# Optimization experiments

Measured on AMD Instinct MI355X. Metric: run time of the kernel, lower is better.

The kernel has to match this reference:

```python
import jax, jax.numpy as jnp
from jax import lax
import numpy as np

B = 32  # batch


def _conv(x, w, b, pad):
    # x: [B,Cin,H,W], w: [Cout,Cin,kh,kw], b: [Cout]
    y = lax.conv_general_dilated(x, w, window_strides=(1, 1), padding=pad,
                                 dimension_numbers=("NCHW", "OIHW", "NCHW"))
    return y + b[None, :, None, None]


def setup_inputs() -> dict:
    keys = jax.random.split(jax.random.key(0), 16)
    ki = iter(keys)
    f32 = jnp.float32

    def W(shape):
        return jax.random.normal(next(ki), shape, f32) * 0.05

    return {
        "x": jax.random.normal(next(ki), (B, 64, 64), f32),
        # 64 independent spatial convs per stage, each Conv2d(Cin,31,(64,3))
        "W1": W((64, 31, 1, 64, 3)),  "b1": jnp.zeros((64, 31), f32),
        "W2": W((64, 31, 31, 64, 3)), "b2": jnp.zeros((64, 31), f32),
        "W3": W((64, 31, 31, 64, 3)), "b3": jnp.zeros((64, 31), f32),
        # 2 edge spectral stacks: Conv(2,64,9)->ReLU->Conv(64,32,1)->ReLU->Conv(32,1,5)
        "We1a": W((2, 64, 2, 9, 9)),  "be1a": jnp.zeros((2, 64), f32),
        "We1b": W((2, 32, 64, 1, 1)), "be1b": jnp.zeros((2, 32), f32),
        "We1c": W((2, 1, 32, 5, 5)),  "be1c": jnp.zeros((2, 1), f32),
        # 29 interior spectral stacks: Conv(3,64,9)->ReLU->Conv(64,32,1)->ReLU->Conv(32,1,5)
        "We2a": W((29, 64, 3, 9, 9)),  "be2a": jnp.zeros((29, 64), f32),
        "We2b": W((29, 32, 64, 1, 1)), "be2b": jnp.zeros((29, 32), f32),
        "We2c": W((29, 1, 32, 5, 5)),  "be2c": jnp.zeros((29, 1), f32),
    }


def _spatial(inp, Ws, bs):
    # inp: [B,Cin,64,64]; Ws: [64,31,Cin,64,3]; bs: [64,31]
    def one(w, b):
        return jax.nn.relu(_conv(inp, w, b, [(0, 0), (1, 1)]))  # [B,31,1,64]
    rows = jax.vmap(one)(Ws, bs)            # [64,B,31,1,64]; row i = output line i
    return jnp.transpose(rows[:, :, :, 0, :], (1, 2, 0, 3))  # [B,31,64,64]


def _spectral(xin, wa, ba, wb, bb, wc, bc):
    h = jax.nn.relu(_conv(xin, wa, ba, [(4, 4), (4, 4)]))
    h = jax.nn.relu(_conv(h, wb, bb, [(0, 0), (0, 0)]))
    return _conv(h, wc, bc, [(2, 2), (2, 2)])[:, 0]  # [B,64,64]


def reference(x, W1, b1, W2, b2, W3, b3,
              We1a, be1a, We1b, be1b, We1c, be1c,
              We2a, be2a, We2b, be2b, We2c, be2c):
    xb = x[:, None]                         # [B,1,64,64]
    s1 = _spatial(xb, W1, b1)               # [B,31,64,64]
    s2 = _spatial(s1, W2, b2)
    s3 = _spatial(s2, W3, b3)

    # edge bands 0 and 30 use 2-channel slices
    edge_in = jnp.stack([s3[:, 0:2], s3[:, 29:31]])   # [2,B,2,64,64]
    edge = jax.vmap(_spectral)(edge_in, We1a, be1a, We1b, be1b, We1c, be1c)  # [2,B,64,64]

    # interior bands 1..29 use sliding 3-channel slices
    idx = jnp.arange(29)[:, None] + jnp.arange(3)[None, :]  # [29,3]
    mid_in = jnp.transpose(s3[:, idx], (1, 0, 2, 3, 4))     # [29,B,3,64,64]
    mid = jax.vmap(_spectral)(mid_in, We2a, be2a, We2b, be2b, We2c, be2c)  # [29,B,64,64]

    recon = jnp.concatenate(
        [edge[0][:, None], jnp.transpose(mid, (1, 0, 2, 3)), edge[1][:, None]], axis=1)
    out = s3 + recon                        # [B,31,64,64]
    # torch: .transpose(3,1).transpose(2,1) == permute(0,2,3,1)
    return jnp.transpose(out, (0, 2, 3, 1))  # [B,64,64,31]
```

## Files before the change

kernel.cpp:

```cpp
#include <hip/hip_runtime.h>
#include <hip/hip_bf16.h>
#include <stdint.h>

typedef unsigned short u16;
typedef unsigned int   u32;
typedef __attribute__((ext_vector_type(8))) short bf16x8;
typedef __attribute__((ext_vector_type(4))) float f32x4;

__device__ __forceinline__ float us2f(u16 u){ return __uint_as_float(((u32)u)<<16); }
__device__ __forceinline__ float lo2f(u32 w){ return __uint_as_float(w<<16); }
__device__ __forceinline__ float hi2f(u32 w){ return __uint_as_float(w & 0xffff0000u); }
__device__ __forceinline__ u16 f2us(float f){
  u32 u = __float_as_uint(f);
  u32 r = (u + 0x7FFFu + ((u>>16)&1u)) >> 16;
  return (u16)r;
}
__device__ __forceinline__ u32 pk2(float a, float b){ return (u32)f2us(a) | ((u32)f2us(b)<<16); }

__global__ __launch_bounds__(256) void k_prep_x(const float* __restrict__ x, u16* __restrict__ xT){
  __shared__ float tile[64][65];
  const int b = blockIdx.x, t = threadIdx.x;
  #pragma unroll
  for (int q=0;q<4;q++){
    int idx = q*256 + t, r = idx>>4, w4 = (idx&15)*4;
    float4 v = *(const float4*)&x[((size_t)b*64 + r)*64 + w4];
    tile[r][w4]=v.x; tile[r][w4+1]=v.y; tile[r][w4+2]=v.z; tile[r][w4+3]=v.w;
  }
  __syncthreads();
  #pragma unroll
  for (int q=0;q<2;q++){
    int idx = q*256 + t, w = idx>>3, rc = idx&7;
    uint4 o;
    o.x = pk2(tile[rc*8+0][w], tile[rc*8+1][w]);
    o.y = pk2(tile[rc*8+2][w], tile[rc*8+3][w]);
    o.z = pk2(tile[rc*8+4][w], tile[rc*8+5][w]);
    o.w = pk2(tile[rc*8+6][w], tile[rc*8+7][w]);
    *(uint4*)&xT[((size_t)b*64 + w)*64 + rc*8] = o;
  }
}

__global__ __launch_bounds__(256) void k_prep_w(const float* __restrict__ W,
        u16* __restrict__ Wp, int CI){
  __shared__ float rowW[5952];
  const int h = blockIdx.x, i = blockIdx.y, t = threadIdx.x;
  for (int idx=t; idx<1488; idx+=256){
    int o = idx/48, j4 = (idx - o*48)*4;
    float4 v = *(const float4*)&W[ (((size_t)h*31 + o)*CI + i)*192 + j4 ];
    *(float4*)&rowW[o*192 + j4] = v;
  }
  __syncthreads();
  for (int idx=t; idx<768; idx+=256){
    int dw = idx>>8, rem = idx&255, o = rem>>3, rc = rem&7;
    uint4 ov = {0,0,0,0};
    if (o < 31){
      const float* s = &rowW[o*192 + dw];
      ov.x = pk2(s[(rc*8+0)*3], s[(rc*8+1)*3]);
      ov.y = pk2(s[(rc*8+2)*3], s[(rc*8+3)*3]);
      ov.z = pk2(s[(rc*8+4)*3], s[(rc*8+5)*3]);
      ov.w = pk2(s[(rc*8+6)*3], s[(rc*8+7)*3]);
    }
    *(uint4*)&Wp[ ((((size_t)h*CI + i)*3 + dw)*32 + o)*64 + rc*8 ] = ov;
  }
}

__global__ __launch_bounds__(128) void k_spatial2(const u16* __restrict__ inT_g,
        const u16* __restrict__ Wp, const float* __restrict__ bias,
        float* __restrict__ outF, u16* __restrict__ outT, int CI, int mode){
  __shared__ __align__(16) u16 inT[2][66*72];
  const int t    = threadIdx.x;
  const int wv   = t>>6;
  const int lane = t&63;
  const int l15  = lane&15;
  const int quad = lane>>4;
  const int b    = blockIdx.x;
  const int hg   = blockIdx.y;
  const int h    = hg*2 + wv;

  if (t < 72){
    inT[0][t] = 0; inT[0][65*72 + t] = 0;
    inT[1][t] = 0; inT[1][65*72 + t] = 0;
  }

  f32x4 acc[2][4];
  #pragma unroll
  for (int n=0;n<2;n++)
    #pragma unroll
    for (int ms=0;ms<4;ms++) acc[n][ms] = (f32x4){0.f,0.f,0.f,0.f};

  const uint4* srcb = (const uint4*)(inT_g + (size_t)b*CI*4096);

  uint4 pf[4];
  #pragma unroll
  for (int q=0;q<4;q++) pf[q] = srcb[q*128 + t];

  for (int i=0;i<CI;i++){
    u16* L = inT[i&1];
    #pragma unroll
    for (int q=0;q<4;q++){
      int idx = q*128 + t, row = idx>>3, ch = idx&7;
      *(uint4*)&L[(row+1)*72 + ch*8] = pf[q];
    }
    if (i+1 < CI){
      const uint4* src = srcb + (size_t)(i+1)*512;
      #pragma unroll
      for (int q=0;q<4;q++) pf[q] = src[q*128 + t];
    }
    const u16* wbase = Wp + ((size_t)h*CI + i)*3*32*64;
    bf16x8 bfr[2][3][2];
    #pragma unroll
    for (int dw=0;dw<3;dw++)
      #pragma unroll
      for (int n=0;n<2;n++)
        #pragma unroll
        for (int kh=0;kh<2;kh++)
          bfr[kh][dw][n] = *(const bf16x8*)&wbase[(dw*32 + n*16 + l15)*64 + kh*32 + quad*8];
    asm volatile("s_waitcnt lgkmcnt(0)" ::: "memory");
    __builtin_amdgcn_s_barrier();
    __builtin_amdgcn_sched_barrier(0);
    #pragma unroll
    for (int kh=0; kh<2; kh++){
      #pragma unroll
      for (int dw=0; dw<3; dw++){
        bf16x8 afr[4];
        #pragma unroll
        for (int ms=0;ms<4;ms++)
          afr[ms] = *(const bf16x8*)&L[(ms*16 + l15 + dw)*72 + kh*32 + quad*8];
        #pragma unroll
        for (int n=0;n<2;n++)
          #pragma unroll
          for (int ms=0;ms<4;ms++)
            acc[n][ms] = __builtin_amdgcn_mfma_f32_16x16x32_bf16(afr[ms], bfr[kh][dw][n], acc[n][ms], 0,0,0);
      }
    }
  }
  #pragma unroll
  for (int n=0;n<2;n++){
    int o = n*16 + l15;
    if (o < 31){
      float bv = bias[h*31 + o];
      if (mode == 0){
        #pragma unroll
        for (int ms=0;ms<4;ms++){
          size_t base = (((size_t)b*31 + o)*64 + h)*64 + ms*16 + quad*4;
          #pragma unroll
          for (int reg=0;reg<4;reg++)
            outF[base + reg] = fmaxf(acc[n][ms][reg] + bv, 0.f);
        }
      } else {
        #pragma unroll
        for (int ms=0;ms<4;ms++){
          int w0 = ms*16 + quad*4;
          #pragma unroll
          for (int reg=0;reg<4;reg++)
            outT[ (((size_t)b*31 + o)*64 + (w0+reg))*64 + h ] = f2us(fmaxf(acc[n][ms][reg] + bv, 0.f));
        }
      }
    }
  }
}

__global__ __launch_bounds__(256) void k_prep(
    const float* __restrict__ We1a, const float* __restrict__ We2a,
    const float* __restrict__ We1b, const float* __restrict__ We2b,
    u16* __restrict__ waP, u16* __restrict__ wbP){
  int t = blockIdx.x*256 + threadIdx.x;
  if (t < 17856){
    int g = t/576, rem = t - g*576, dx = rem>>6, c = rem&63;
    int C; const float* wa;
    if (g==0)      { C=2; wa = We1a; }
    else if (g==30){ C=2; wa = We1a + 64*2*81; }
    else           { C=3; wa = We2a + (size_t)(g-1)*64*3*81; }
    const float* wrow = wa + (size_t)c*C*81;
    u16* dst = waP + ((size_t)(g*9 + dx)*64 + c)*40;
    int Kr = C*9;
    for (int k=0;k<40;k++){
      u16 v = 0;
      if (k < Kr) v = f2us(wrow[k*9 + dx]);
      dst[k] = v;
    }
  } else if (t < 17856 + 992){
    int u = t - 17856; int g = u>>5, c2 = u&31;
    const float* wb;
    if (g==0)      wb = We1b;
    else if (g==30) wb = We1b + 32*64;
    else            wb = We2b + (size_t)(g-1)*32*64;
    u16* dst = wbP + ((size_t)g*32 + c2)*72;
    for (int k=0;k<64;k++) dst[k] = f2us(wb[c2*64 + k]);
    for (int k=64;k<72;k++) dst[k] = 0;
  }
}

__global__ __launch_bounds__(256) void k_spec_ab(
    const float* __restrict__ s3,
    const u16* __restrict__ waP, const u16* __restrict__ wbP,
    const float* __restrict__ be1a, const float* __restrict__ be1b,
    const float* __restrict__ be2a, const float* __restrict__ be2b,
    u16* __restrict__ hb, int g0){
  __shared__ __align__(16) unsigned char smem[36864];
  u16* colT = (u16*)smem;
  u16* haT  = (u16*)smem;
  u16* hbL  = (u16*)smem;

  const int t = threadIdx.x;
  const int yo = blockIdx.x, b = blockIdx.y;
  const int gl = blockIdx.z;
  const int g  = g0 + gl;
  const int y0 = yo*4;
  const int wv = t>>6, lane = t&63, l15 = lane&15, quad = lane>>4;

  int C, cb; const float *ba, *bb;
  if (g==0)      { C=2; cb=0;  ba=be1a;           bb=be1b;        }
  else if (g==30){ C=2; cb=29; ba=be1a+64;        bb=be1b+32;     }
  else           { C=3; cb=g-1; ba=be2a+(size_t)(g-1)*64; bb=be2b+(size_t)(g-1)*32; }

  {
    uint4 z = {0,0,0,0};
    uint4* c4 = (uint4*)colT;
    #pragma unroll
    for (int j=0;j<6;j++){ int idx = j*256 + t; if (idx < 1440) c4[idx] = z; }
  }
  __syncthreads();

  for (int idx=t; idx<576; idx+=256){
    int i = idx/192, rem = idx-192*i;
    int x4 = rem/12, yext = rem - x4*12;
    int yrow = y0 + yext - 4;
    if (i < C && yrow >= 0 && yrow < 64){
      float4 v = *(const float4*)&s3[ (((size_t)b*31 + cb + i)*64 + yrow)*64 + x4*4 ];
      u16 q0=f2us(v.x), q1=f2us(v.y), q2=f2us(v.z), q3=f2us(v.w);
      #pragma unroll
      for (int yl=0; yl<4; yl++){
        int dy = yext - yl;
        if (dy >= 0 && dy < 9){
          int k = i*9 + dy;
          int base = (yl*72 + x4*4 + 4)*40 + k;
          colT[base      ] = q0;
          colT[base + 40 ] = q1;
          colT[base + 80 ] = q2;
          colT[base + 120] = q3;
        }
      }
    }
  }
  __syncthreads();

  f32x4 acc[4][4];
  #pragma unroll
  for (int yl=0;yl<4;yl++)
    #pragma unroll
    for (int nf=0;nf<4;nf++) acc[yl][nf] = (f32x4){0.f,0.f,0.f,0.f};

  const u16* waPg = waP + (size_t)g*9*64*40;
  #pragma unroll
  for (int dx=0; dx<9; dx++){
    bf16x8 af[4];
    #pragma unroll
    for (int yl=0;yl<4;yl++)
      af[yl] = *(const bf16x8*)&colT[(yl*72 + wv*16 + l15 + dx)*40 + quad*8];
    #pragma unroll
    for (int nf=0;nf<4;nf++){
      bf16x8 bfr = *(const bf16x8*)&waPg[(dx*64 + nf*16 + l15)*40 + quad*8];
      #pragma unroll
      for (int yl=0;yl<4;yl++)
        acc[yl][nf] = __builtin_amdgcn_mfma_f32_16x16x32_bf16(af[yl], bfr, acc[yl][nf], 0,0,0);
    }
  }
  __syncthreads();

  #pragma unroll
  for (int nf=0;nf<4;nf++){
    float bav = ba[nf*16 + l15];
    #pragma unroll
    for (int yl=0;yl<4;yl++){
      int px = yl*64 + wv*16 + quad*4;
      #pragma unroll
      for (int reg=0;reg<4;reg++)
        haT[(px+reg)*72 + nf*16 + l15] = f2us(fmaxf(acc[yl][nf][reg] + bav, 0.f));
    }
  }
  __syncthreads();

  bf16x8 a2[2][4];
  #pragma unroll
  for (int kh=0; kh<2; kh++)
    #pragma unroll
    for (int j=0;j<4;j++)
      a2[kh][j] = *(const bf16x8*)&haT[((wv*4+j)*16 + l15)*72 + kh*32 + quad*8];
  __syncthreads();

  const u16* wb_g = wbP + (size_t)g*32*72;
  f32x4 acc2[4][2];
  #pragma unroll
  for (int j=0;j<4;j++){ acc2[j][0] = (f32x4){0.f,0.f,0.f,0.f}; acc2[j][1] = (f32x4){0.f,0.f,0.f,0.f}; }
  #pragma unroll
  for (int kh=0; kh<2; kh++){
    #pragma unroll
    for (int nf=0;nf<2;nf++){
      bf16x8 b2 = *(const bf16x8*)&wb_g[(nf*16 + l15)*72 + kh*32 + quad*8];
      #pragma unroll
      for (int j=0;j<4;j++)
        acc2[j][nf] = __builtin_amdgcn_mfma_f32_16x16x32_bf16(a2[kh][j], b2, acc2[j][nf], 0,0,0);
    }
  }
  #pragma unroll
  for (int nf=0;nf<2;nf++){
    float bbv = bb[nf*16 + l15];
    #pragma unroll
    for (int j=0;j<4;j++){
      int px = (wv*4+j)*16 + quad*4;
      uint2 pw;
      pw.x = pk2(fmaxf(acc2[j][nf][0] + bbv, 0.f), fmaxf(acc2[j][nf][1] + bbv, 0.f));
      pw.y = pk2(fmaxf(acc2[j][nf][2] + bbv, 0.f), fmaxf(acc2[j][nf][3] + bbv, 0.f));
      *(uint2*)&hbL[(nf*16+l15)*296 + px] = pw;
    }
  }
  __syncthreads();

  {
    int c2 = t>>3, xq = t&7;
    size_t base = (((size_t)gl*32 + b)*32 + c2)*4096 + (size_t)yo*256 + xq*32;
    #pragma unroll
    for (int q=0;q<4;q++)
      *(uint4*)&hb[base + q*8] = *(const uint4*)&hbL[c2*296 + xq*32 + q*8];
  }
}

__global__ __launch_bounds__(256) void k_spec_c(
    const u16* __restrict__ hb, const float* __restrict__ We1c, const float* __restrict__ be1c,
    const float* __restrict__ We2c, const float* __restrict__ be2c,
    float* __restrict__ rec, int g0){
  __shared__ __align__(16) unsigned char smemC[58368 + 3200];
  u16*   hbT  = (u16*)smemC;
  float* wcL  = (float*)(smemC + 58368);
  float* redc = (float*)smemC;
  const int t  = threadIdx.x;
  const int y0 = blockIdx.x*8;
  const int b  = blockIdx.y;
  const int gl = blockIdx.z;
  const int g  = g0 + gl;
  const float *wc, *bc;
  if (g==0)      { wc = We1c;             bc = be1c;       }
  else if (g==30){ wc = We1c + 800;       bc = be1c + 1;   }
  else           { wc = We2c + (g-1)*800; bc = be2c + (g-1); }

  for (int idx=t; idx<384; idx+=256){
    int c2 = idx/12, row = idx - c2*12;
    u32* d32 = (u32*)&hbT[(size_t)(c2*12 + row)*76];
    d32[0]  = 0;
    d32[33] = 0;
    u32* di = d32 + 1;
    int yg = y0 - 2 + row;
    if (yg >= 0 && yg < 64){
      const uint4* srcp = (const uint4*)&hb[ (((size_t)gl*32 + b)*32 + c2)*4096 + (size_t)yg*64 ];
      #pragma unroll
      for (int q=0;q<8;q++){
        uint4 v = srcp[q];
        di[q*4+0]=v.x; di[q*4+1]=v.y; di[q*4+2]=v.z; di[q*4+3]=v.w;
      }
    } else {
      #pragma unroll
      for (int q=0;q<32;q++) di[q] = 0;
    }
  }
  for (int idx=t; idx<800; idx+=256) wcL[idx] = wc[idx];
  __syncthreads();

  const int xt = t&7, yq = (t>>3)&7, cqt = t>>6;
  const int x0 = xt*8;
  float acc[8];
  #pragma unroll
  for (int p=0;p<8;p++) acc[p]=0.f;
  for (int c2 = cqt*8; c2 < cqt*8+8; c2++){
    #pragma unroll
    for (int dy=0;dy<5;dy++){
      const uint2* hp = (const uint2*)&hbT[(c2*12 + yq+dy)*76 + x0];
      uint2 v0 = hp[0], v1 = hp[1], v2 = hp[2];
      float h[12];
      h[0]=lo2f(v0.x); h[1]=hi2f(v0.x); h[2]=lo2f(v0.y); h[3]=hi2f(v0.y);
      h[4]=lo2f(v1.x); h[5]=hi2f(v1.x); h[6]=lo2f(v1.y); h[7]=hi2f(v1.y);
      h[8]=lo2f(v2.x); h[9]=hi2f(v2.x); h[10]=lo2f(v2.y); h[11]=hi2f(v2.y);
      #pragma unroll
      for (int dx=0;dx<5;dx++){
        float wv = wcL[c2*25 + dy*5 + dx];
        #pragma unroll
        for (int p=0;p<8;p++) acc[p] = fmaf(h[p+dx], wv, acc[p]);
      }
    }
  }
  __syncthreads();
  int slot = yq*8 + xt;
  if (cqt >= 2){
    #pragma unroll
    for (int p=0;p<8;p++) redc[((cqt-2)*64 + slot)*8 + p] = acc[p];
  }
  __syncthreads();
  if (cqt < 2){
    #pragma unroll
    for (int p=0;p<8;p++) acc[p] += redc[(cqt*64 + slot)*8 + p];
  }
  __syncthreads();
  if (cqt == 1){
    #pragma unroll
    for (int p=0;p<8;p++) redc[slot*8 + p] = acc[p];
  }
  __syncthreads();
  if (cqt == 0){
    float bcv = bc[0];
    size_t base = (((size_t)g*32 + b)*64 + (y0+yq))*64 + x0;
    #pragma unroll
    for (int p=0;p<8;p++) rec[base+p] = acc[p] + redc[slot*8 + p] + bcv;
  }
}

__global__ __launch_bounds__(256) void k_final(const float* __restrict__ s3,
        const float* __restrict__ rec, float* __restrict__ out){
  __shared__ float tile[31][65];
  const int t = threadIdx.x;
  const int y = blockIdx.x & 63;
  const int b = blockIdx.x >> 6;
  for (int idx=t; idx<1984; idx+=256){
    int o = idx>>6, x = idx&63;
    tile[o][x] = s3[ (((size_t)b*31+o)*64 + y)*64 + x ]
               + rec[ (((size_t)o*32+b)*64 + y)*64 + x ];
  }
  __syncthreads();
  size_t base = ((size_t)b*4096 + (size_t)y*64)*31;
  for (int idx=t; idx<1984; idx+=256){
    int x = idx/31, o = idx-31*x;
    out[base+idx] = tile[o][x];
  }
}

extern "C" void kernel_launch(void* const* d_in, const int* in_sizes, int n_in,
                              void* d_out, int out_size, void* d_ws, size_t ws_size,
                              hipStream_t stream){
  const float* x    = (const float*)d_in[0];
  const float* W1   = (const float*)d_in[1];
  const float* b1   = (const float*)d_in[2];
  const float* W2   = (const float*)d_in[3];
  const float* b2   = (const float*)d_in[4];
  const float* W3   = (const float*)d_in[5];
  const float* b3   = (const float*)d_in[6];
  const float* We1a = (const float*)d_in[7];
  const float* be1a = (const float*)d_in[8];
  const float* We1b = (const float*)d_in[9];
  const float* be1b = (const float*)d_in[10];
  const float* We1c = (const float*)d_in[11];
  const float* be1c = (const float*)d_in[12];
  const float* We2a = (const float*)d_in[13];
  const float* be2a = (const float*)d_in[14];
  const float* We2b = (const float*)d_in[15];
  const float* be2b = (const float*)d_in[16];
  const float* We2c = (const float*)d_in[17];
  const float* be2c = (const float*)d_in[18];
  float* out = (float*)d_out;

  char* ws = (char*)d_ws;
  float* s3  = (float*)(ws);
  u16*   Wp  = (u16*)(ws + 16777216);
  u16*   xT  = (u16*)(ws + 44040192);
  float* rec = (float*)(ws + 16777216);
  u16*   hb  = (u16*)(ws + 33030144);

  u16* s1T = (u16*)((char*)d_out);
  u16* s2T = (u16*)((char*)d_out + 8126464);
  u16* waP = (u16*)((char*)d_out);
  u16* wbP = (u16*)((char*)d_out + 1440000);

  dim3 bs(256);
  dim3 bsp(128), gsp(32,32);
  k_prep_x<<<dim3(32),bs,0,stream>>>(x, xT);
  k_prep_w<<<dim3(64,1),bs,0,stream>>>(W1, Wp, 1);
  k_spatial2<<<gsp,bsp,0,stream>>>(xT,  Wp, b1, nullptr, s1T, 1, 1);
  k_prep_w<<<dim3(64,31),bs,0,stream>>>(W2, Wp, 31);
  k_spatial2<<<gsp,bsp,0,stream>>>(s1T, Wp, b2, nullptr, s2T, 31, 1);
  k_prep_w<<<dim3(64,31),bs,0,stream>>>(W3, Wp, 31);
  k_spatial2<<<gsp,bsp,0,stream>>>(s2T, Wp, b3, s3, nullptr, 31, 0);

  k_prep<<<dim3(74),bs,0,stream>>>(We1a, We2a, We1b, We2b, waP, wbP);

  int batch = 8;
  if (ws_size > 33030144ull){
    size_t m = (ws_size - 33030144ull) / 8388608ull;
    if (m < 1) m = 1;
    if (m > 8) m = 8;
    batch = (int)m;
  }
  for (int g0=0; g0<31; g0+=batch){
    int c = 31 - g0; if (c > batch) c = batch;
    k_spec_ab<<<dim3(16,32,c),bs,0,stream>>>(s3, waP, wbP, be1a, be1b, be2a, be2b, hb, g0);
    k_spec_c <<<dim3(8,32,c),bs,0,stream>>>(hb, We1c,be1c,We2c,be2c, rec, g0);
  }
  k_final<<<dim3(2048),bs,0,stream>>>(s3, rec, out);
}
```

Baseline: 1.043 ms.

## Widen spatial conv blocks, prefetch weights, coalesce stores via separate transpose

The spatial conv kernel now runs 4 waves per block (256 threads) over a 1D grid with an XCD-aware mapping of blocks to output rows and batches. Weight fragments for the next input channel are double-buffered in registers so their global loads overlap the MFMA work. The scattered per-element transposed bf16 stores are replaced by packed row-major stores, and a new LDS-swizzled transpose kernel between stages produces the layout the next stage expects. The price is two extra kernel launches plus extra global round-trips for the transposes, and higher register pressure from the doubled weight fragments.

```diff
diff --git a/kernel.cpp b/kernel.cpp
--- a/kernel.cpp
+++ b/kernel.cpp
@@ -63,7 +63,34 @@
   }
 }
 
-__global__ __launch_bounds__(128) void k_spatial2(const u16* __restrict__ inT_g,
+__global__ __launch_bounds__(256) void k_tr(const u16* __restrict__ in, u16* __restrict__ outp){
+  __shared__ u16 tile[64*72];
+  const int b = blockIdx.x, o = blockIdx.y, t = threadIdx.x;
+  const uint4* src = (const uint4*)(in + ((size_t)b*31 + o)*4096);
+  #pragma unroll
+  for (int q=0;q<2;q++){
+    int idx = q*256 + t, hh = idx>>3, u = idx&7;
+    *(uint4*)&tile[hh*72 + ((u ^ ((hh>>3)&7))*8)] = src[idx];
+  }
+  __syncthreads();
+  u16* dst = outp + ((size_t)b*31 + o)*4096;
+  #pragma unroll
+  for (int q=0;q<2;q++){
+    int idx = q*256 + t, w = idx>>3, hc = (idx&7)*8;
+    u32 ow[4];
+    #pragma unroll
+    for (int j=0;j<4;j++){
+      int h0 = hc + j*2, h1 = h0 + 1;
+      u16 a = tile[h0*72 + (((w>>3) ^ ((h0>>3)&7))*8) + (w&7)];
+      u16 bb= tile[h1*72 + (((w>>3) ^ ((h1>>3)&7))*8) + (w&7)];
+      ow[j] = (u32)a | ((u32)bb<<16);
+    }
+    uint4 ov = {ow[0], ow[1], ow[2], ow[3]};
+    *(uint4*)&dst[(size_t)w*64 + hc] = ov;
+  }
+}
+
+__global__ __launch_bounds__(256) void k_spatial2(const u16* __restrict__ inT_g,
         const u16* __restrict__ Wp, const float* __restrict__ bias,
         float* __restrict__ outF, u16* __restrict__ outT, int CI, int mode){
   __shared__ __align__(16) u16 inT[2][66*72];
@@ -72,9 +99,12 @@
   const int lane = t&63;
   const int l15  = lane&15;
   const int quad = lane>>4;
-  const int b    = blockIdx.x;
-  const int hg   = blockIdx.y;
-  const int h    = hg*2 + wv;
+  const int wg  = blockIdx.x;
+  const int xcd = wg & 7;
+  const int li  = wg >> 3;
+  const int hg  = xcd*2 + (li>>5);
+  const int b   = li & 31;
+  const int h   = hg*4 + wv;
 
   if (t < 72){
     inT[0][t] = 0; inT[0][65*72 + t] = 0;
@@ -88,32 +118,39 @@
     for (int ms=0;ms<4;ms++) acc[n][ms] = (f32x4){0.f,0.f,0.f,0.f};
 
   const uint4* srcb = (const uint4*)(inT_g + (size_t)b*CI*4096);
-
-  uint4 pf[4];
-  #pragma unroll
-  for (int q=0;q<4;q++) pf[q] = srcb[q*128 + t];
-
-  for (int i=0;i<CI;i++){
+  const u16*   wrow = Wp + (size_t)h*CI*3*32*64;
+
+  uint4 pf[2];
+  #pragma unroll
+  for (int q=0;q<2;q++) pf[q] = srcb[q*256 + t];
+  bf16x8 bA[2][3][2], bB[2][3][2];
+  #pragma unroll
+  for (int dw=0;dw<3;dw++)
+    #pragma unroll
+    for (int n=0;n<2;n++)
+      #pragma unroll
+      for (int kh=0;kh<2;kh++)
+        bA[kh][dw][n] = *(const bf16x8*)&wrow[(dw*32 + n*16 + l15)*64 + kh*32 + quad*8];
+
+  auto body = [&](bf16x8 (&bcur)[2][3][2], bf16x8 (&bnext)[2][3][2], int i){
     u16* L = inT[i&1];
     #pragma unroll
-    for (int q=0;q<4;q++){
-      int idx = q*128 + t, row = idx>>3, ch = idx&7;
+    for (int q=0;q<2;q++){
+      int idx = q*256 + t, row = idx>>3, ch = idx&7;
       *(uint4*)&L[(row+1)*72 + ch*8] = pf[q];
     }
-    if (i+1 < CI){
-      const uint4* src = srcb + (size_t)(i+1)*512;
-      #pragma unroll
-      for (int q=0;q<4;q++) pf[q] = src[q*128 + t];
-    }
-    const u16* wbase = Wp + ((size_t)h*CI + i)*3*32*64;
-    bf16x8 bfr[2][3][2];
+    int inext = (i+1 < CI) ? (i+1) : (CI-1);
+    const uint4* src = srcb + (size_t)inext*512;
+    #pragma unroll
+    for (int q=0;q<2;q++) pf[q] = src[q*256 + t];
+    const u16* wbase = wrow + (size_t)inext*3*32*64;
     #pragma unroll
     for (int dw=0;dw<3;dw++)
       #pragma unroll
       for (int n=0;n<2;n++)
         #pragma unroll
         for (int kh=0;kh<2;kh++)
-          bfr[kh][dw][n] = *(const bf16x8*)&wbase[(dw*32 + n*16 + l15)*64 + kh*32 + quad*8];
+          bnext[kh][dw][n] = *(const bf16x8*)&wbase[(dw*32 + n*16 + l15)*64 + kh*32 + quad*8];
     asm volatile("s_waitcnt lgkmcnt(0)" ::: "memory");
     __builtin_amdgcn_s_barrier();
     __builtin_amdgcn_sched_barrier(0);
@@ -129,10 +166,17 @@
         for (int n=0;n<2;n++)
           #pragma unroll
           for (int ms=0;ms<4;ms++)
-            acc[n][ms] = __builtin_amdgcn_mfma_f32_16x16x32_bf16(afr[ms], bfr[kh][dw][n], acc[n][ms], 0,0,0);
+            acc[n][ms] = __builtin_amdgcn_mfma_f32_16x16x32_bf16(afr[ms], bcur[kh][dw][n], acc[n][ms], 0,0,0);
       }
     }
-  }
+  };
+
+  int i = 0;
+  while (true){
+    body(bA, bB, i); if (++i >= CI) break;
+    body(bB, bA, i); if (++i >= CI) break;
+  }
+
   #pragma unroll
   for (int n=0;n<2;n++){
     int o = n*16 + l15;
@@ -149,10 +193,10 @@
       } else {
         #pragma unroll
         for (int ms=0;ms<4;ms++){
-          int w0 = ms*16 + quad*4;
-          #pragma unroll
-          for (int reg=0;reg<4;reg++)
-            outT[ (((size_t)b*31 + o)*64 + (w0+reg))*64 + h ] = f2us(fmaxf(acc[n][ms][reg] + bv, 0.f));
+          uint2 pw;
+          pw.x = pk2(fmaxf(acc[n][ms][0] + bv, 0.f), fmaxf(acc[n][ms][1] + bv, 0.f));
+          pw.y = pk2(fmaxf(acc[n][ms][2] + bv, 0.f), fmaxf(acc[n][ms][3] + bv, 0.f));
+          *(uint2*)&outT[ (((size_t)b*31 + o)*64 + h)*64 + ms*16 + quad*4 ] = pw;
         }
       }
     }
@@ -462,20 +506,22 @@
   float* rec = (float*)(ws + 16777216);
   u16*   hb  = (u16*)(ws + 33030144);
 
-  u16* s1T = (u16*)((char*)d_out);
-  u16* s2T = (u16*)((char*)d_out + 8126464);
+  u16* bufA = (u16*)((char*)d_out);
+  u16* bufB = (u16*)((char*)d_out + 8126464);
   u16* waP = (u16*)((char*)d_out);
   u16* wbP = (u16*)((char*)d_out + 1440000);
 
   dim3 bs(256);
-  dim3 bsp(128), gsp(32,32);
+  dim3 gsp(512), gtr(32,31);
   k_prep_x<<<dim3(32),bs,0,stream>>>(x, xT);
   k_prep_w<<<dim3(64,1),bs,0,stream>>>(W1, Wp, 1);
-  k_spatial2<<<gsp,bsp,0,stream>>>(xT,  Wp, b1, nullptr, s1T, 1, 1);
+  k_spatial2<<<gsp,bs,0,stream>>>(xT,  Wp, b1, nullptr, bufA, 1, 1);
+  k_tr<<<gtr,bs,0,stream>>>(bufA, bufB);
   k_prep_w<<<dim3(64,31),bs,0,stream>>>(W2, Wp, 31);
-  k_spatial2<<<gsp,bsp,0,stream>>>(s1T, Wp, b2, nullptr, s2T, 31, 1);
+  k_spatial2<<<gsp,bs,0,stream>>>(bufB, Wp, b2, nullptr, bufA, 31, 1);
+  k_tr<<<gtr,bs,0,stream>>>(bufA, bufB);
   k_prep_w<<<dim3(64,31),bs,0,stream>>>(W3, Wp, 31);
-  k_spatial2<<<gsp,bsp,0,stream>>>(s2T, Wp, b3, s3, nullptr, 31, 0);
+  k_spatial2<<<gsp,bs,0,stream>>>(bufB, Wp, b3, s3, nullptr, 31, 0);
 
   k_prep<<<dim3(74),bs,0,stream>>>(We1a, We2a, We1b, We2b, waP, wbP);
 
```

Measured after the change: 994.5 us. 1.05x faster.
